# Performance work log

Measured on AMD Instinct MI355X. Metric: run time of the kernel, lower is better.

The kernel has to match this reference:

```python
import jax, jax.numpy as jnp
import numpy as np

N = 100000
E = 1600000
D = 64
EPS = 1e-5


def setup_inputs() -> dict:
    key = jax.random.key(0)
    ks = jax.random.split(key, 16)
    x = jax.random.normal(ks[0], (N, D), dtype=jnp.float32)
    edge_index = jax.random.randint(ks[1], (2, E), 0, N, dtype=jnp.int64)
    s = 1.0 / np.sqrt(D)
    params = {
        'W1': jax.random.uniform(ks[2], (D, D), jnp.float32, -s, s),
        'b1': jnp.zeros((D,), jnp.float32),
        'g1': jnp.ones((D,), jnp.float32),
        'be1': jnp.zeros((D,), jnp.float32),
        'W2': jax.random.uniform(ks[3], (D, D), jnp.float32, -s, s),
        'b2': jnp.zeros((D,), jnp.float32),
        'g2': jnp.ones((D,), jnp.float32),
        'be2': jnp.zeros((D,), jnp.float32),
        'W3': jax.random.uniform(ks[4], (D, D), jnp.float32, -s, s),
        'b3': jnp.zeros((D,), jnp.float32),
    }
    return {'x': x, 'edge_index': edge_index, **params}


def _gcn_norm(edge_index):
    # add self-loops, symmetric normalization (PyG GCNConv default)
    loop = jnp.arange(N, dtype=edge_index.dtype)
    src = jnp.concatenate([edge_index[0], loop])  # [E+N]
    dst = jnp.concatenate([edge_index[1], loop])
    deg = jax.ops.segment_sum(jnp.ones_like(src, dtype=jnp.float32), dst, num_segments=N)
    dinv = jnp.where(deg > 0, jax.lax.rsqrt(deg), 0.0)
    norm = dinv[src] * dinv[dst]  # [E+N]
    return src, dst, norm


def _gcn_conv(x, src, dst, norm, W, b):
    h = x @ W                        # [N, D] transform first (PyG order)
    msg = h[src] * norm[:, None]     # gather + scale  [E+N, D]
    out = jax.ops.segment_sum(msg, dst, num_segments=N)  # scatter-add
    return out + b


def _bn(x, g, b):
    # BatchNorm1d over nodes, batch statistics (training-mode math)
    m = jnp.mean(x, axis=0)
    v = jnp.var(x, axis=0)
    return g * (x - m) * jax.lax.rsqrt(v + EPS) + b


def reference(x, edge_index, W1, b1, g1, be1, W2, b2, g2, be2, W3, b3):
    src, dst, norm = _gcn_norm(edge_index)
    h = _gcn_conv(x, src, dst, norm, W1, b1)
    h = jax.nn.relu(_bn(h, g1, be1))
    h = _gcn_conv(h, src, dst, norm, W2, b2)
    h = jax.nn.relu(_bn(h, g2, be2))
    h = _gcn_conv(h, src, dst, norm, W3, b3)
    return h
```

## Files before the change

### kernel.cpp

```cpp
#include <hip/hip_runtime.h>
#include <hip/hip_bf16.h>


#define FD 64
#define EPSF 1e-5f

#define NBUCK 256
#define BSHIFT 9
#define BWID 512
#define SLOTS 28
#define P1_EDGES 4096

typedef __attribute__((ext_vector_type(8))) short bf16x8;
typedef __attribute__((ext_vector_type(4))) float f32x4;

__device__ __forceinline__ ushort f2bf_bits(float f) {
  __hip_bfloat16 h = __float2bfloat16(f);
  return *(ushort*)&h;
}
__device__ __forceinline__ unsigned packbf(float lo, float hi) {
  return (unsigned)f2bf_bits(lo) | ((unsigned)f2bf_bits(hi) << 16);
}

__global__ __launch_bounds__(256) void init_kernel(const int* __restrict__ ei,
                                                   int* __restrict__ flag,
                                                   int* __restrict__ bhist,
                                                   float* __restrict__ stats1,
                                                   float* __restrict__ stats2) {
  int t = threadIdx.x;
  bhist[t] = 0;
  if (t < 128) {
    stats1[t] = 0.f;
    stats2[t] = 0.f;
  }
  if (t < 64) {
    int v = ei[2 * t + 1];
    unsigned long long nz = __ballot(v != 0);
    if (t == 0) *flag = (nz == 0ull) ? 1 : 0;
  }
}

__global__ __launch_bounds__(256) void hist_kernel(const int* __restrict__ ei, int E,
                                                   const int* __restrict__ flag,
                                                   int* __restrict__ bhist) {
  __shared__ int h[NBUCK];
  const int tid = threadIdx.x;
  h[tid] = 0;
  __syncthreads();
  const int is64 = *flag;
  const int base = blockIdx.x * P1_EDGES;
#pragma unroll 1
  for (int k = 0; k < P1_EDGES / 256; ++k) {
    int e = base + k * 256 + tid;
    if (e < E) {
      int d = is64 ? ei[2 * (E + e)] : ei[E + e];
      atomicAdd(&h[d >> BSHIFT], 1);
    }
  }
  __syncthreads();
  if (h[tid]) atomicAdd(&bhist[tid], h[tid]);
}

__global__ __launch_bounds__(256) void bscan_kernel(const int* __restrict__ bhist,
                                                    int* __restrict__ bbase,
                                                    int* __restrict__ bcur) {
  __shared__ int lds[NBUCK];
  int t = threadIdx.x;
  int v = bhist[t];
  lds[t] = v;
  __syncthreads();
  for (int off = 1; off < NBUCK; off <<= 1) {
    int tv = (t >= off) ? lds[t - off] : 0;
    __syncthreads();
    lds[t] += tv;
    __syncthreads();
  }
  int ex = lds[t] - v;
  bbase[t] = ex;
  bcur[t] = ex;
}

__global__ __launch_bounds__(256) void fill1_kernel(const int* __restrict__ ei, int E,
                                                    const int* __restrict__ flag,
                                                    int* __restrict__ bcur,
                                                    int2* __restrict__ stage) {
  __shared__ int2 sbuf[NBUCK][SLOTS];
  __shared__ int scnt[NBUCK];
  __shared__ int sbase[NBUCK];
  const int tid = threadIdx.x;
  scnt[tid] = 0;
  __syncthreads();
  const int is64 = *flag;
  const int base = blockIdx.x * P1_EDGES;
#pragma unroll 1
  for (int k = 0; k < P1_EDGES / 256; ++k) {
    int e = base + k * 256 + tid;
    if (e < E) {
      int s = is64 ? ei[2 * e] : ei[e];
      int d = is64 ? ei[2 * (E + e)] : ei[E + e];
      int b = d >> BSHIFT;
      int pos = atomicAdd(&scnt[b], 1);
      if (pos < SLOTS) {
        sbuf[b][pos] = make_int2(s, d);
      } else {
        stage[atomicAdd(&bcur[b], 1)] = make_int2(s, d);
      }
    }
  }
  __syncthreads();
  {
    int c = scnt[tid];
    if (c > SLOTS) c = SLOTS;
    scnt[tid] = c;
    sbase[tid] = c ? atomicAdd(&bcur[tid], c) : 0;
  }
  __syncthreads();
  for (int idx = tid; idx < NBUCK * SLOTS; idx += 256) {
    int b = idx / SLOTS, sl = idx - b * SLOTS;
    if (sl < scnt[b]) stage[sbase[b] + sl] = sbuf[b][sl];
  }
}

__global__ __launch_bounds__(256) void degscan_kernel(const int2* __restrict__ stage,
                                                      const int* __restrict__ bbase,
                                                      const int* __restrict__ bcur,
                                                      int* __restrict__ rowptr,
                                                      int* __restrict__ cursor,
                                                      float* __restrict__ dinv,
                                                      int N, int nB) {
  __shared__ int h[BWID];
  __shared__ int ps[256];
  const int b = blockIdx.x;
  const int tid = threadIdx.x;
  h[tid] = 0;
  h[tid + 256] = 0;
  __syncthreads();
  const int lo = bbase[b], hi = bcur[b];
  for (int i = lo + tid; i < hi; i += 256)
    atomicAdd(&h[stage[i].y - (b << BSHIFT)], 1);
  __syncthreads();
  const int a0 = h[2 * tid], a1 = h[2 * tid + 1];
  ps[tid] = a0 + a1;
  __syncthreads();
  for (int off = 1; off < 256; off <<= 1) {
    int v = (tid >= off) ? ps[tid - off] : 0;
    __syncthreads();
    ps[tid] += v;
    __syncthreads();
  }
  const int excl = ps[tid] - (a0 + a1);
  const int n0 = b << BSHIFT;
  const int na = n0 + 2 * tid;
  const int nb2 = na + 1;
  if (na < N) {
    int r = lo + excl;
    rowptr[na] = r;
    cursor[na] = r;
    dinv[na] = rsqrtf((float)(a0 + 1));
  }
  if (nb2 < N) {
    int r = lo + excl + a0;
    rowptr[nb2] = r;
    cursor[nb2] = r;
    dinv[nb2] = rsqrtf((float)(a1 + 1));
  }
  if (b == nB - 1 && tid == 255) rowptr[N] = lo + ps[255];
}

__global__ __launch_bounds__(256) void fill2_kernel(const int2* __restrict__ stage,
                                                    const int* __restrict__ bbase,
                                                    const int* __restrict__ bcur,
                                                    int* __restrict__ cursor,
                                                    const float* __restrict__ dinv,
                                                    int2* __restrict__ colw) {
  const int b = blockIdx.x >> 1;
  const int half = blockIdx.x & 1;
  const int lo = bbase[b];
  const int hi = bcur[b];
  for (int i = lo + half * 256 + threadIdx.x; i < hi; i += 512) {
    int2 sd = stage[i];
    int slot = atomicAdd(&cursor[sd.y], 1);
    colw[slot] = make_int2(sd.x, __float_as_int(dinv[sd.x] * dinv[sd.y]));
  }
}

__global__ __launch_bounds__(256) void deg_atomic_kernel(const int* __restrict__ ei, int E,
                                                         const int* __restrict__ flag,
                                                         int* __restrict__ deg) {
  int e = blockIdx.x * 256 + threadIdx.x;
  if (e >= E) return;
  const int is64 = *flag;
  int d = is64 ? ei[2 * (E + e)] : ei[E + e];
  atomicAdd(&deg[d], 1);
}
__global__ __launch_bounds__(256) void dinv_kernel(const int* __restrict__ deg,
                                                   float* __restrict__ dinv, int N) {
  int i = blockIdx.x * 256 + threadIdx.x;
  if (i < N) dinv[i] = rsqrtf((float)(deg[i] + 1));
}
__global__ __launch_bounds__(1024) void scan1_kernel(const int* __restrict__ deg,
                                                     int* __restrict__ rowptr,
                                                     int* __restrict__ partial, int N) {
  __shared__ int lds[1024];
  int i = blockIdx.x * 1024 + threadIdx.x;
  int v = (i < N) ? deg[i] : 0;
  lds[threadIdx.x] = v;
  __syncthreads();
  for (int off = 1; off < 1024; off <<= 1) {
    int t = (threadIdx.x >= (unsigned)off) ? lds[threadIdx.x - off] : 0;
    __syncthreads();
    lds[threadIdx.x] += t;
    __syncthreads();
  }
  if (i < N) rowptr[i + 1] = lds[threadIdx.x];
  if (threadIdx.x == 1023) partial[blockIdx.x] = lds[1023];
}
__global__ __launch_bounds__(128) void scan2_kernel(int* __restrict__ partial, int B) {
  __shared__ int lds[128];
  int t = threadIdx.x;
  int v = (t < B) ? partial[t] : 0;
  lds[t] = v;
  __syncthreads();
  for (int off = 1; off < 128; off <<= 1) {
    int tv = (t >= off) ? lds[t - off] : 0;
    __syncthreads();
    lds[t] += tv;
    __syncthreads();
  }
  if (t < B) partial[t] = lds[t] - v;
}
__global__ __launch_bounds__(1024) void scan3_kernel(const int* __restrict__ deg,
                                                     int* __restrict__ rowptr,
                                                     const int* __restrict__ partial,
                                                     int* __restrict__ cursor, int N) {
  int i = blockIdx.x * 1024 + threadIdx.x;
  if (i < N) {
    int r = rowptr[i + 1] + partial[blockIdx.x];
    rowptr[i + 1] = r;
    cursor[i] = r - deg[i];
    if (i == 0) rowptr[0] = 0;
  }
}
__global__ __launch_bounds__(256) void fill_direct_kernel(const int* __restrict__ ei, int E,
                                                          const int* __restrict__ flag,
                                                          const float* __restrict__ dinv,
                                                          int* __restrict__ cursor,
                                                          int2* __restrict__ colw) {
  int e = blockIdx.x * 256 + threadIdx.x;
  if (e >= E) return;
  const int is64 = *flag;
  int s = is64 ? ei[2 * e] : ei[e];
  int d = is64 ? ei[2 * (E + e)] : ei[E + e];
  int slot = atomicAdd(&cursor[d], 1);
  colw[slot] = make_int2(s, __float_as_int(dinv[s] * dinv[d]));
}

__global__ __launch_bounds__(256) void cast_kernel(const float* __restrict__ in,
                                                   ushort* __restrict__ out, int total) {
  int i = (blockIdx.x * 256 + threadIdx.x) * 4;
  if (i >= total) return;
  float4 v = *(const float4*)(in + i);
  ushort4 o;
  o.x = f2bf_bits(v.x);
  o.y = f2bf_bits(v.y);
  o.z = f2bf_bits(v.z);
  o.w = f2bf_bits(v.w);
  *(ushort4*)(out + i) = o;
}

__global__ __launch_bounds__(256) void bnrelu_kernel(ushort* __restrict__ T,
                                                     const float* __restrict__ stats,
                                                     const float* __restrict__ g,
                                                     const float* __restrict__ be,
                                                     int N) {
  __shared__ float sa[FD], sc[FD];
  if (threadIdx.x < FD) {
    const float invN = 1.0f / (float)N;
    float m = stats[threadIdx.x] * invN;
    float v = stats[FD + threadIdx.x] * invN - m * m;
    float r = rsqrtf(v + EPSF);
    float a = g[threadIdx.x] * r;
    sa[threadIdx.x] = a;
    sc[threadIdx.x] = be[threadIdx.x] - m * a;
  }
  __syncthreads();
  const int idx = (blockIdx.x * 256 + threadIdx.x) * 8;
  if (idx >= N * FD) return;
  const int f0 = idx & (FD - 1);
  uint4 v = *(const uint4*)(T + idx);
  float h0 = __uint_as_float(v.x << 16);
  float h1 = __uint_as_float(v.x & 0xffff0000u);
  float h2 = __uint_as_float(v.y << 16);
  float h3 = __uint_as_float(v.y & 0xffff0000u);
  float h4 = __uint_as_float(v.z << 16);
  float h5 = __uint_as_float(v.z & 0xffff0000u);
  float h6 = __uint_as_float(v.w << 16);
  float h7 = __uint_as_float(v.w & 0xffff0000u);
  h0 = fmaxf(fmaf(sa[f0 + 0], h0, sc[f0 + 0]), 0.f);
  h1 = fmaxf(fmaf(sa[f0 + 1], h1, sc[f0 + 1]), 0.f);
  h2 = fmaxf(fmaf(sa[f0 + 2], h2, sc[f0 + 2]), 0.f);
  h3 = fmaxf(fmaf(sa[f0 + 3], h3, sc[f0 + 3]), 0.f);
  h4 = fmaxf(fmaf(sa[f0 + 4], h4, sc[f0 + 4]), 0.f);
  h5 = fmaxf(fmaf(sa[f0 + 5], h5, sc[f0 + 5]), 0.f);
  h6 = fmaxf(fmaf(sa[f0 + 6], h6, sc[f0 + 6]), 0.f);
  h7 = fmaxf(fmaf(sa[f0 + 7], h7, sc[f0 + 7]), 0.f);
  uint4 o;
  o.x = packbf(h0, h1);
  o.y = packbf(h2, h3);
  o.z = packbf(h4, h5);
  o.w = packbf(h6, h7);
  *(uint4*)(T + idx) = o;
}

__global__ __launch_bounds__(256) void agg_kernel(const ushort* __restrict__ H,
                                                  const int* __restrict__ rowptr,
                                                  const int2* __restrict__ colw,
                                                  const float* __restrict__ dinv,
                                                  ushort* __restrict__ out, int N) {
  const int lane = threadIdx.x & 63;
  const int wid = threadIdx.x >> 6;
  const int grp = lane >> 4;
  const int sg = (lane >> 3) & 1;
  const int fl8 = lane & 7;
  const int dst = (blockIdx.x * 4 + wid) * 4 + grp;
  const bool live = dst < N;
  const int dc = live ? dst : N - 1;

  const int e0 = rowptr[dc];
  const int e1 = live ? rowptr[dc + 1] : e0;

  float acc[4][8];
#pragma unroll
  for (int u = 0; u < 4; ++u)
#pragma unroll
    for (int j = 0; j < 8; ++j) acc[u][j] = 0.f;

  for (int base = e0; __any(base < e1); base += 8) {
#pragma unroll
    for (int u = 0; u < 4; ++u) {
      const int ee = base + 2 * u + sg;
      const bool valid = ee < e1;
      const int idx = valid ? ee : 0;
      const int2 cw = colw[idx];
      const float w = valid ? __int_as_float(cw.y) : 0.f;
      const uint4 uv = *(const uint4*)(H + (size_t)cw.x * FD + fl8 * 8);
      acc[u][0] = fmaf(w, __uint_as_float(uv.x << 16), acc[u][0]);
      acc[u][1] = fmaf(w, __uint_as_float(uv.x & 0xffff0000u), acc[u][1]);
      acc[u][2] = fmaf(w, __uint_as_float(uv.y << 16), acc[u][2]);
      acc[u][3] = fmaf(w, __uint_as_float(uv.y & 0xffff0000u), acc[u][3]);
      acc[u][4] = fmaf(w, __uint_as_float(uv.z << 16), acc[u][4]);
      acc[u][5] = fmaf(w, __uint_as_float(uv.z & 0xffff0000u), acc[u][5]);
      acc[u][6] = fmaf(w, __uint_as_float(uv.w << 16), acc[u][6]);
      acc[u][7] = fmaf(w, __uint_as_float(uv.w & 0xffff0000u), acc[u][7]);
    }
  }

  float r[8];
#pragma unroll
  for (int j = 0; j < 8; ++j)
    r[j] = (acc[0][j] + acc[1][j]) + (acc[2][j] + acc[3][j]);
#pragma unroll
  for (int j = 0; j < 8; ++j) r[j] += __shfl_xor(r[j], 8);

  const float di = dinv[dc];
  const float dsq = di * di;
  const uint4 sv = *(const uint4*)(H + (size_t)dc * FD + fl8 * 8);
  r[0] = fmaf(dsq, __uint_as_float(sv.x << 16), r[0]);
  r[1] = fmaf(dsq, __uint_as_float(sv.x & 0xffff0000u), r[1]);
  r[2] = fmaf(dsq, __uint_as_float(sv.y << 16), r[2]);
  r[3] = fmaf(dsq, __uint_as_float(sv.y & 0xffff0000u), r[3]);
  r[4] = fmaf(dsq, __uint_as_float(sv.z << 16), r[4]);
  r[5] = fmaf(dsq, __uint_as_float(sv.z & 0xffff0000u), r[5]);
  r[6] = fmaf(dsq, __uint_as_float(sv.w << 16), r[6]);
  r[7] = fmaf(dsq, __uint_as_float(sv.w & 0xffff0000u), r[7]);

  if (live && sg == 0) {
    uint4 o;
    o.x = packbf(r[0], r[1]);
    o.y = packbf(r[2], r[3]);
    o.z = packbf(r[4], r[5]);
    o.w = packbf(r[6], r[7]);
    *(uint4*)(out + (size_t)dst * FD + fl8 * 8) = o;
  }
}

template <bool BF16OUT>
__global__ __launch_bounds__(256) void gemm_mfma_kernel(const ushort* __restrict__ A,
                                                        const float* __restrict__ W,
                                                        const float* __restrict__ bias,
                                                        ushort* __restrict__ outb,
                                                        float* __restrict__ outf,
                                                        float* __restrict__ stats, int N) {
  const int lane = threadIdx.x & 63;
  const int wid = threadIdx.x >> 6;
  const int lo = lane & 15;
  const int hi = lane >> 4;

  __shared__ float sred[128];
  if (BF16OUT) {
    if (threadIdx.x < 128) sred[threadIdx.x] = 0.f;
    __syncthreads();
  }

  bf16x8 bfrag[2][4];
#pragma unroll
  for (int kk = 0; kk < 2; ++kk)
#pragma unroll
    for (int nt = 0; nt < 4; ++nt)
#pragma unroll
      for (int j = 0; j < 8; ++j) {
        int k = kk * 32 + hi * 8 + j;
        bfrag[kk][nt][j] = (short)f2bf_bits(W[k * FD + nt * 16 + lo]);
      }

  float bl[4];
#pragma unroll
  for (int nt = 0; nt < 4; ++nt) bl[nt] = bias[nt * 16 + lo];

  float s1[4] = {0.f, 0.f, 0.f, 0.f};
  float s2[4] = {0.f, 0.f, 0.f, 0.f};

  const int TILES = (N + 15) / 16;
  const int stride = gridDim.x * 4;
  for (int tile = blockIdx.x * 4 + wid; tile < TILES; tile += stride) {
    const int row0 = tile * 16;
    const int ar = min(row0 + lo, N - 1);
    const ushort* ap = A + (size_t)ar * FD + hi * 8;
    bf16x8 a0 = *(const bf16x8*)ap;
    bf16x8 a1 = *(const bf16x8*)(ap + 32);

    f32x4 acc[4] = {{0.f, 0.f, 0.f, 0.f},
                    {0.f, 0.f, 0.f, 0.f},
                    {0.f, 0.f, 0.f, 0.f},
                    {0.f, 0.f, 0.f, 0.f}};
#pragma unroll
    for (int nt = 0; nt < 4; ++nt) {
      acc[nt] = __builtin_amdgcn_mfma_f32_16x16x32_bf16(a0, bfrag[0][nt], acc[nt], 0, 0, 0);
      acc[nt] = __builtin_amdgcn_mfma_f32_16x16x32_bf16(a1, bfrag[1][nt], acc[nt], 0, 0, 0);
    }

#pragma unroll
    for (int nt = 0; nt < 4; ++nt) {
#pragma unroll
      for (int r = 0; r < 4; ++r) {
        int row = row0 + hi * 4 + r;
        if (row < N) {
          float o = acc[nt][r] + bl[nt];
          if (BF16OUT) {
            outb[(size_t)row * FD + nt * 16 + lo] = f2bf_bits(o);
            s1[nt] += o;
            s2[nt] += o * o;
          } else {
            outf[(size_t)row * FD + nt * 16 + lo] = o;
          }
        }
      }
    }
  }

  if (BF16OUT) {
#pragma unroll
    for (int nt = 0; nt < 4; ++nt) {
      atomicAdd(&sred[nt * 16 + lo], s1[nt]);
      atomicAdd(&sred[64 + nt * 16 + lo], s2[nt]);
    }
    __syncthreads();
    if (threadIdx.x < 128) atomicAdd(&stats[threadIdx.x], sred[threadIdx.x]);
  }
}

extern "C" void kernel_launch(void* const* d_in, const int* in_sizes, int n_in,
                              void* d_out, int out_size, void* d_ws, size_t ws_size,
                              hipStream_t stream) {
  const float* x = (const float*)d_in[0];
  const int* ei = (const int*)d_in[1];
  const float* W1 = (const float*)d_in[2];
  const float* b1 = (const float*)d_in[3];
  const float* g1 = (const float*)d_in[4];
  const float* be1 = (const float*)d_in[5];
  const float* W2 = (const float*)d_in[6];
  const float* b2 = (const float*)d_in[7];
  const float* g2 = (const float*)d_in[8];
  const float* be2 = (const float*)d_in[9];
  const float* W3 = (const float*)d_in[10];
  const float* b3 = (const float*)d_in[11];

  const int N = in_sizes[0] / FD;
  const int E = in_sizes[1] / 2;
  const int nB = (N + BWID - 1) >> BSHIFT;

  char* p = (char*)d_ws;
  auto alloc = [&](size_t bytes) {
    char* r = p;
    p += (bytes + 255) & ~(size_t)255;
    return r;
  };
  int* flag = (int*)alloc(4);
  float* stats1 = (float*)alloc(128 * 4);
  float* stats2 = (float*)alloc(128 * 4);
  int* partial = (int*)alloc(128 * 4);
  int* bhist = (int*)alloc(NBUCK * 4);
  int* bbase = (int*)alloc(NBUCK * 4);
  int* bcur = (int*)alloc(NBUCK * 4);
  int* deg = (int*)alloc((size_t)N * 4);
  float* dinv = (float*)alloc((size_t)N * 4);
  int* rowptr = (int*)alloc((size_t)(N + 1) * 4);
  int* cursor = (int*)alloc((size_t)N * 4);
  int2* colw = (int2*)alloc((size_t)E * 8);
  ushort* T0 = (ushort*)alloc((size_t)N * FD * 2);
  ushort* T1 = (ushort*)alloc((size_t)N * FD * 2);
  size_t base_need = (size_t)(p - (char*)d_ws);
  int2* stage = (int2*)alloc((size_t)E * 8);
  size_t full_need = (size_t)(p - (char*)d_ws);
  const bool two_phase =
      ((ws_size == 0) || (ws_size >= full_need)) && (N <= NBUCK * BWID);
  (void)base_need;

  const int NB = (N + 1023) / 1024;
  const int EB = (E + P1_EDGES - 1) / P1_EDGES;

  init_kernel<<<1, 256, 0, stream>>>(ei, flag, bhist, stats1, stats2);

  if (two_phase) {
    hist_kernel<<<EB, 256, 0, stream>>>(ei, E, flag, bhist);
    bscan_kernel<<<1, NBUCK, 0, stream>>>(bhist, bbase, bcur);
    fill1_kernel<<<EB, 256, 0, stream>>>(ei, E, flag, bcur, stage);
    degscan_kernel<<<nB, 256, 0, stream>>>(stage, bbase, bcur, rowptr, cursor, dinv, N,
                                           nB);
    fill2_kernel<<<2 * nB, 256, 0, stream>>>(stage, bbase, bcur, cursor, dinv, colw);
  } else {
    hipMemsetAsync(deg, 0, (size_t)N * 4, stream);
    deg_atomic_kernel<<<(E + 255) / 256, 256, 0, stream>>>(ei, E, flag, deg);
    dinv_kernel<<<(N + 255) / 256, 256, 0, stream>>>(deg, dinv, N);
    scan1_kernel<<<NB, 1024, 0, stream>>>(deg, rowptr, partial, N);
    scan2_kernel<<<1, 128, 0, stream>>>(partial, NB);
    scan3_kernel<<<NB, 1024, 0, stream>>>(deg, rowptr, partial, cursor, N);
    fill_direct_kernel<<<(E + 255) / 256, 256, 0, stream>>>(ei, E, flag, dinv, cursor,
                                                            colw);
  }

  const int aggGrid = (N + 15) / 16;
  const int castGrid = (N * FD / 4 + 255) / 256;
  const int bnGrid = (N * FD / 8 + 255) / 256;
  const int TILES = (N + 15) / 16;
  const int gemmGrid = (TILES + 15) / 16;

  cast_kernel<<<castGrid, 256, 0, stream>>>(x, T0, N * FD);
  agg_kernel<<<aggGrid, 256, 0, stream>>>(T0, rowptr, colw, dinv, T1, N);
  gemm_mfma_kernel<true><<<gemmGrid, 256, 0, stream>>>(T1, W1, b1, T0, nullptr, stats1, N);

  bnrelu_kernel<<<bnGrid, 256, 0, stream>>>(T0, stats1, g1, be1, N);
  agg_kernel<<<aggGrid, 256, 0, stream>>>(T0, rowptr, colw, dinv, T1, N);
  gemm_mfma_kernel<true><<<gemmGrid, 256, 0, stream>>>(T1, W2, b2, T0, nullptr, stats2, N);

  bnrelu_kernel<<<bnGrid, 256, 0, stream>>>(T0, stats2, g2, be2, N);
  agg_kernel<<<aggGrid, 256, 0, stream>>>(T0, rowptr, colw, dinv, T1, N);
  gemm_mfma_kernel<false><<<gemmGrid, 256, 0, stream>>>(T1, W3, b3, nullptr,
                                                        (float*)d_out, nullptr, N);
}
```

Baseline: 308.9 us.

## Bucket destination nodes by degree class to balance aggregation wavefronts

Adds a degree-class histogram in degscan and a permutation kernel that groups nodes with similar in-degree (8 classes of degree/8). The aggregation kernel now walks nodes through this permutation, so the four nodes sharing a wavefront have similar edge counts and fewer lanes sit idle in the __any loop. The aggregation grid also becomes a capped grid-stride loop. The cost is an extra kernel, an indirection load per node, and output writes scattered in the original node order, which loses some locality.

```diff
diff --git a/kernel.cpp b/kernel.cpp
--- a/kernel.cpp
+++ b/kernel.cpp
@@ -26,13 +26,15 @@
                                                    int* __restrict__ flag,
                                                    int* __restrict__ bhist,
                                                    float* __restrict__ stats1,
-                                                   float* __restrict__ stats2) {
+                                                   float* __restrict__ stats2,
+                                                   int* __restrict__ classCnt) {
   int t = threadIdx.x;
   bhist[t] = 0;
   if (t < 128) {
     stats1[t] = 0.f;
     stats2[t] = 0.f;
   }
+  if (t < 8) classCnt[t] = 0;
   if (t < 64) {
     int v = ei[2 * t + 1];
     unsigned long long nz = __ballot(v != 0);
@@ -127,13 +129,16 @@
                                                       int* __restrict__ rowptr,
                                                       int* __restrict__ cursor,
                                                       float* __restrict__ dinv,
+                                                      int* __restrict__ classCnt,
                                                       int N, int nB) {
   __shared__ int h[BWID];
   __shared__ int ps[256];
+  __shared__ int ch[8];
   const int b = blockIdx.x;
   const int tid = threadIdx.x;
   h[tid] = 0;
   h[tid + 256] = 0;
+  if (tid < 8) ch[tid] = 0;
   __syncthreads();
   const int lo = bbase[b], hi = bcur[b];
   for (int i = lo + tid; i < hi; i += 256)
@@ -157,14 +162,18 @@
     rowptr[na] = r;
     cursor[na] = r;
     dinv[na] = rsqrtf((float)(a0 + 1));
+    atomicAdd(&ch[min(a0 >> 3, 7)], 1);
   }
   if (nb2 < N) {
     int r = lo + excl + a0;
     rowptr[nb2] = r;
     cursor[nb2] = r;
     dinv[nb2] = rsqrtf((float)(a1 + 1));
+    atomicAdd(&ch[min(a1 >> 3, 7)], 1);
   }
   if (b == nB - 1 && tid == 255) rowptr[N] = lo + ps[255];
+  __syncthreads();
+  if (tid < 8 && ch[tid]) atomicAdd(&classCnt[tid], ch[tid]);
 }
 
 __global__ __launch_bounds__(256) void fill2_kernel(const int2* __restrict__ stage,
@@ -172,7 +181,17 @@
                                                     const int* __restrict__ bcur,
                                                     int* __restrict__ cursor,
                                                     const float* __restrict__ dinv,
-                                                    int2* __restrict__ colw) {
+                                                    int2* __restrict__ colw,
+                                                    const int* __restrict__ classCnt,
+                                                    int* __restrict__ classCur) {
+  if (blockIdx.x == 0 && threadIdx.x == 0) {
+    int s = 0;
+#pragma unroll
+    for (int c = 0; c < 8; ++c) {
+      classCur[c] = s;
+      s += classCnt[c];
+    }
+  }
   const int b = blockIdx.x >> 1;
   const int half = blockIdx.x & 1;
   const int lo = bbase[b];
@@ -182,6 +201,32 @@
     int slot = atomicAdd(&cursor[sd.y], 1);
     colw[slot] = make_int2(sd.x, __float_as_int(dinv[sd.x] * dinv[sd.y]));
   }
+}
+
+__global__ __launch_bounds__(256) void permfill_kernel(const int* __restrict__ rowptr,
+                                                       int* __restrict__ classCur,
+                                                       int* __restrict__ perm, int N) {
+  __shared__ int lc[8], lbase[8];
+  const int tid = threadIdx.x;
+  if (tid < 8) lc[tid] = 0;
+  __syncthreads();
+  const int n = blockIdx.x * 256 + tid;
+  int c = 0, sl = 0;
+  const bool live = n < N;
+  if (live) {
+    int deg = rowptr[n + 1] - rowptr[n];
+    c = min(deg >> 3, 7);
+    sl = atomicAdd(&lc[c], 1);
+  }
+  __syncthreads();
+  if (tid < 8) lbase[tid] = lc[tid] ? atomicAdd(&classCur[tid], lc[tid]) : 0;
+  __syncthreads();
+  if (live) perm[lbase[c] + sl] = n;
+}
+
+__global__ __launch_bounds__(256) void identperm_kernel(int* __restrict__ perm, int N) {
+  int n = blockIdx.x * 256 + threadIdx.x;
+  if (n < N) perm[n] = n;
 }
 
 __global__ __launch_bounds__(256) void deg_atomic_kernel(const int* __restrict__ ei, int E,
@@ -316,71 +361,75 @@
                                                   const int* __restrict__ rowptr,
                                                   const int2* __restrict__ colw,
                                                   const float* __restrict__ dinv,
+                                                  const int* __restrict__ perm,
                                                   ushort* __restrict__ out, int N) {
   const int lane = threadIdx.x & 63;
   const int wid = threadIdx.x >> 6;
   const int grp = lane >> 4;
   const int sg = (lane >> 3) & 1;
   const int fl8 = lane & 7;
-  const int dst = (blockIdx.x * 4 + wid) * 4 + grp;
-  const bool live = dst < N;
-  const int dc = live ? dst : N - 1;
-
-  const int e0 = rowptr[dc];
-  const int e1 = live ? rowptr[dc + 1] : e0;
-
-  float acc[4][8];
-#pragma unroll
-  for (int u = 0; u < 4; ++u)
-#pragma unroll
-    for (int j = 0; j < 8; ++j) acc[u][j] = 0.f;
-
-  for (int base = e0; __any(base < e1); base += 8) {
-#pragma unroll
-    for (int u = 0; u < 4; ++u) {
-      const int ee = base + 2 * u + sg;
-      const bool valid = ee < e1;
-      const int idx = valid ? ee : 0;
-      const int2 cw = colw[idx];
-      const float w = valid ? __int_as_float(cw.y) : 0.f;
-      const uint4 uv = *(const uint4*)(H + (size_t)cw.x * FD + fl8 * 8);
-      acc[u][0] = fmaf(w, __uint_as_float(uv.x << 16), acc[u][0]);
-      acc[u][1] = fmaf(w, __uint_as_float(uv.x & 0xffff0000u), acc[u][1]);
-      acc[u][2] = fmaf(w, __uint_as_float(uv.y << 16), acc[u][2]);
-      acc[u][3] = fmaf(w, __uint_as_float(uv.y & 0xffff0000u), acc[u][3]);
-      acc[u][4] = fmaf(w, __uint_as_float(uv.z << 16), acc[u][4]);
-      acc[u][5] = fmaf(w, __uint_as_float(uv.z & 0xffff0000u), acc[u][5]);
-      acc[u][6] = fmaf(w, __uint_as_float(uv.w << 16), acc[u][6]);
-      acc[u][7] = fmaf(w, __uint_as_float(uv.w & 0xffff0000u), acc[u][7]);
-    }
-  }
-
-  float r[8];
-#pragma unroll
-  for (int j = 0; j < 8; ++j)
-    r[j] = (acc[0][j] + acc[1][j]) + (acc[2][j] + acc[3][j]);
-#pragma unroll
-  for (int j = 0; j < 8; ++j) r[j] += __shfl_xor(r[j], 8);
-
-  const float di = dinv[dc];
-  const float dsq = di * di;
-  const uint4 sv = *(const uint4*)(H + (size_t)dc * FD + fl8 * 8);
-  r[0] = fmaf(dsq, __uint_as_float(sv.x << 16), r[0]);
-  r[1] = fmaf(dsq, __uint_as_float(sv.x & 0xffff0000u), r[1]);
-  r[2] = fmaf(dsq, __uint_as_float(sv.y << 16), r[2]);
-  r[3] = fmaf(dsq, __uint_as_float(sv.y & 0xffff0000u), r[3]);
-  r[4] = fmaf(dsq, __uint_as_float(sv.z << 16), r[4]);
-  r[5] = fmaf(dsq, __uint_as_float(sv.z & 0xffff0000u), r[5]);
-  r[6] = fmaf(dsq, __uint_as_float(sv.w << 16), r[6]);
-  r[7] = fmaf(dsq, __uint_as_float(sv.w & 0xffff0000u), r[7]);
-
-  if (live && sg == 0) {
-    uint4 o;
-    o.x = packbf(r[0], r[1]);
-    o.y = packbf(r[2], r[3]);
-    o.z = packbf(r[4], r[5]);
-    o.w = packbf(r[6], r[7]);
-    *(uint4*)(out + (size_t)dst * FD + fl8 * 8) = o;
+  const int nquad = (N + 3) >> 2;
+
+  for (int q = blockIdx.x * 4 + wid; q < nquad; q += gridDim.x * 4) {
+    const int di_ = q * 4 + grp;
+    const bool live = di_ < N;
+    const int node = perm[live ? di_ : N - 1];
+    const int e0 = rowptr[node];
+    const int e1 = live ? rowptr[node + 1] : e0;
+
+    float acc[4][8];
+#pragma unroll
+    for (int u = 0; u < 4; ++u)
+#pragma unroll
+      for (int j = 0; j < 8; ++j) acc[u][j] = 0.f;
+
+    for (int base = e0; __any(base < e1); base += 8) {
+#pragma unroll
+      for (int u = 0; u < 4; ++u) {
+        const int ee = base + 2 * u + sg;
+        const bool valid = ee < e1;
+        const int idx = valid ? ee : 0;
+        const int2 cw = colw[idx];
+        const float w = valid ? __int_as_float(cw.y) : 0.f;
+        const uint4 uv = *(const uint4*)(H + (size_t)cw.x * FD + fl8 * 8);
+        acc[u][0] = fmaf(w, __uint_as_float(uv.x << 16), acc[u][0]);
+        acc[u][1] = fmaf(w, __uint_as_float(uv.x & 0xffff0000u), acc[u][1]);
+        acc[u][2] = fmaf(w, __uint_as_float(uv.y << 16), acc[u][2]);
+        acc[u][3] = fmaf(w, __uint_as_float(uv.y & 0xffff0000u), acc[u][3]);
+        acc[u][4] = fmaf(w, __uint_as_float(uv.z << 16), acc[u][4]);
+        acc[u][5] = fmaf(w, __uint_as_float(uv.z & 0xffff0000u), acc[u][5]);
+        acc[u][6] = fmaf(w, __uint_as_float(uv.w << 16), acc[u][6]);
+        acc[u][7] = fmaf(w, __uint_as_float(uv.w & 0xffff0000u), acc[u][7]);
+      }
+    }
+
+    float r[8];
+#pragma unroll
+    for (int j = 0; j < 8; ++j)
+      r[j] = (acc[0][j] + acc[1][j]) + (acc[2][j] + acc[3][j]);
+#pragma unroll
+    for (int j = 0; j < 8; ++j) r[j] += __shfl_xor(r[j], 8);
+
+    const float di = dinv[node];
+    const float dsq = di * di;
+    const uint4 sv = *(const uint4*)(H + (size_t)node * FD + fl8 * 8);
+    r[0] = fmaf(dsq, __uint_as_float(sv.x << 16), r[0]);
+    r[1] = fmaf(dsq, __uint_as_float(sv.x & 0xffff0000u), r[1]);
+    r[2] = fmaf(dsq, __uint_as_float(sv.y << 16), r[2]);
+    r[3] = fmaf(dsq, __uint_as_float(sv.y & 0xffff0000u), r[3]);
+    r[4] = fmaf(dsq, __uint_as_float(sv.z << 16), r[4]);
+    r[5] = fmaf(dsq, __uint_as_float(sv.z & 0xffff0000u), r[5]);
+    r[6] = fmaf(dsq, __uint_as_float(sv.w << 16), r[6]);
+    r[7] = fmaf(dsq, __uint_as_float(sv.w & 0xffff0000u), r[7]);
+
+    if (live && sg == 0) {
+      uint4 o;
+      o.x = packbf(r[0], r[1]);
+      o.y = packbf(r[2], r[3]);
+      o.z = packbf(r[4], r[5]);
+      o.w = packbf(r[6], r[7]);
+      *(uint4*)(out + (size_t)node * FD + fl8 * 8) = o;
+    }
   }
 }
 
@@ -502,10 +551,13 @@
   int* bhist = (int*)alloc(NBUCK * 4);
   int* bbase = (int*)alloc(NBUCK * 4);
   int* bcur = (int*)alloc(NBUCK * 4);
+  int* classCnt = (int*)alloc(8 * 4);
+  int* classCur = (int*)alloc(8 * 4);
   int* deg = (int*)alloc((size_t)N * 4);
   float* dinv = (float*)alloc((size_t)N * 4);
   int* rowptr = (int*)alloc((size_t)(N + 1) * 4);
   int* cursor = (int*)alloc((size_t)N * 4);
+  int* perm = (int*)alloc((size_t)N * 4);
   int2* colw = (int2*)alloc((size_t)E * 8);
   ushort* T0 = (ushort*)alloc((size_t)N * FD * 2);
   ushort* T1 = (ushort*)alloc((size_t)N * FD * 2);
@@ -519,15 +571,17 @@
   const int NB = (N + 1023) / 1024;
   const int EB = (E + P1_EDGES - 1) / P1_EDGES;
 
-  init_kernel<<<1, 256, 0, stream>>>(ei, flag, bhist, stats1, stats2);
+  init_kernel<<<1, 256, 0, stream>>>(ei, flag, bhist, stats1, stats2, classCnt);
 
   if (two_phase) {
     hist_kernel<<<EB, 256, 0, stream>>>(ei, E, flag, bhist);
     bscan_kernel<<<1, NBUCK, 0, stream>>>(bhist, bbase, bcur);
     fill1_kernel<<<EB, 256, 0, stream>>>(ei, E, flag, bcur, stage);
-    degscan_kernel<<<nB, 256, 0, stream>>>(stage, bbase, bcur, rowptr, cursor, dinv, N,
-                                           nB);
-    fill2_kernel<<<2 * nB, 256, 0, stream>>>(stage, bbase, bcur, cursor, dinv, colw);
+    degscan_kernel<<<nB, 256, 0, stream>>>(stage, bbase, bcur, rowptr, cursor, dinv,
+                                           classCnt, N, nB);
+    fill2_kernel<<<2 * nB, 256, 0, stream>>>(stage, bbase, bcur, cursor, dinv, colw,
+                                             classCnt, classCur);
+    permfill_kernel<<<(N + 255) / 256, 256, 0, stream>>>(rowptr, classCur, perm, N);
   } else {
     hipMemsetAsync(deg, 0, (size_t)N * 4, stream);
     deg_atomic_kernel<<<(E + 255) / 256, 256, 0, stream>>>(ei, E, flag, deg);
@@ -537,24 +591,26 @@
     scan3_kernel<<<NB, 1024, 0, stream>>>(deg, rowptr, partial, cursor, N);
     fill_direct_kernel<<<(E + 255) / 256, 256, 0, stream>>>(ei, E, flag, dinv, cursor,
                                                             colw);
-  }
-
-  const int aggGrid = (N + 15) / 16;
+    identperm_kernel<<<(N + 255) / 256, 256, 0, stream>>>(perm, N);
+  }
+
+  const int nquad = (N + 3) / 4;
+  const int aggGrid = min((nquad + 3) / 4, 1664);
   const int castGrid = (N * FD / 4 + 255) / 256;
   const int bnGrid = (N * FD / 8 + 255) / 256;
   const int TILES = (N + 15) / 16;
   const int gemmGrid = (TILES + 15) / 16;
 
   cast_kernel<<<castGrid, 256, 0, stream>>>(x, T0, N * FD);
-  agg_kernel<<<aggGrid, 256, 0, stream>>>(T0, rowptr, colw, dinv, T1, N);
+  agg_kernel<<<aggGrid, 256, 0, stream>>>(T0, rowptr, colw, dinv, perm, T1, N);
   gemm_mfma_kernel<true><<<gemmGrid, 256, 0, stream>>>(T1, W1, b1, T0, nullptr, stats1, N);
 
   bnrelu_kernel<<<bnGrid, 256, 0, stream>>>(T0, stats1, g1, be1, N);
-  agg_kernel<<<aggGrid, 256, 0, stream>>>(T0, rowptr, colw, dinv, T1, N);
+  agg_kernel<<<aggGrid, 256, 0, stream>>>(T0, rowptr, colw, dinv, perm, T1, N);
   gemm_mfma_kernel<true><<<gemmGrid, 256, 0, stream>>>(T1, W2, b2, T0, nullptr, stats2, N);
 
   bnrelu_kernel<<<bnGrid, 256, 0, stream>>>(T0, stats2, g2, be2, N);
-  agg_kernel<<<aggGrid, 256, 0, stream>>>(T0, rowptr, colw, dinv, T1, N);
+  agg_kernel<<<aggGrid, 256, 0, stream>>>(T0, rowptr, colw, dinv, perm, T1, N);
   gemm_mfma_kernel<false><<<gemmGrid, 256, 0, stream>>>(T1, W3, b3, nullptr,
                                                         (float*)d_out, nullptr, N);
 }
```

New measurement: 326.1 us. 1.06x slower.
